# Performance work log

Measured on AMD Instinct MI355X. Metric: run time of the kernel, lower is better.

The kernel has to match this reference:

```python
import jax, jax.numpy as jnp
import numpy as np

N = 100000   # nodes
E = 1600000  # edges (avg degree 16)
DIN, DH, DOUT = 128, 64, 40


def setup_inputs() -> dict:
    key = jax.random.key(0)
    ks = jax.random.split(key, 6)
    x = jax.random.normal(ks[0], (N, DIN), dtype=jnp.float32)
    edge_index = jax.random.randint(ks[1], (2, E), 0, N, dtype=jnp.int32)
    s1 = float(1.0 / np.sqrt(DIN))
    s2 = float(1.0 / np.sqrt(DH))
    W1 = jax.random.uniform(ks[2], (DIN, DH), jnp.float32, -s1, s1)
    b1 = jax.random.uniform(ks[3], (DH,), jnp.float32, -s1, s1)
    W2 = jax.random.uniform(ks[4], (DH, DOUT), jnp.float32, -s2, s2)
    b2 = jax.random.uniform(ks[5], (DOUT,), jnp.float32, -s2, s2)
    return {"x": x, "W1": W1, "b1": b1, "W2": W2, "b2": b2, "edge_index": edge_index}


def _gcn_conv(x, W, b, src, dst):
    """PyG GCNConv: add self-loops, symmetric degree normalization, scatter-add."""
    n = x.shape[0]
    h = x @ W  # [N, F_out] — transform before propagation (PyG order)
    ones = jnp.ones(src.shape[0], dtype=h.dtype)
    deg = jax.ops.segment_sum(ones, dst, num_segments=n) + 1.0  # +1 for self-loop
    dinv = jax.lax.rsqrt(deg)  # deg >= 1, no zero guard needed
    norm = dinv[src] * dinv[dst]  # [E]
    agg = jax.ops.segment_sum(h[src] * norm[:, None], dst, num_segments=n)
    agg = agg + h * (dinv * dinv)[:, None]  # self-loop messages
    return agg + b


def reference(x, W1, b1, W2, b2, edge_index):
    src, dst = edge_index[0], edge_index[1]
    h = jax.nn.relu(_gcn_conv(x, W1, b1, src, dst))
    out = _gcn_conv(h, W2, b2, src, dst)
    return jax.nn.log_softmax(out, axis=1)
```

## Files before the change

### kernel.cpp

```cpp
#include <hip/hip_runtime.h>
#include <hip/hip_fp16.h>
#include <math.h>

#define N_NODES 100000
#define N_EDGES 1600000
#define DIN 128
#define DH 64
#define DOUT 40

#define NB 256
#define BN 391
#define CAP 8192
#define BIN_BLOCKS 256
#define EPB 6250

typedef unsigned short u16;
typedef unsigned int u32;

__device__ inline __half2 u2h(u32 u) {
    union { u32 x; __half2 h; } c; c.x = u; return c.h;
}
__device__ inline u32 h2u(__half2 h) {
    union { __half2 h; u32 x; } c; c.h = h; return c.x;
}


__global__ __launch_bounds__(1024) void k_bin(const int* __restrict__ src,
                                              const int* __restrict__ dst,
                                              int* __restrict__ gcur,
                                              u32* __restrict__ staged) {
    __shared__ int hist[NB];
    __shared__ int base[NB];
    __shared__ int cur[NB];
    int t = threadIdx.x;
    for (int i = t; i < NB; i += 1024) { hist[i] = 0; cur[i] = 0; }
    __syncthreads();
    int e0 = blockIdx.x * EPB;
    int e1 = e0 + EPB; if (e1 > N_EDGES) e1 = N_EDGES;
    for (int e = e0 + t; e < e1; e += 1024)
        atomicAdd(&hist[dst[e] / BN], 1);
    __syncthreads();
    for (int i = t; i < NB; i += 1024) {
        int h = hist[i];
        base[i] = h ? atomicAdd(&gcur[i], h) : 0;
    }
    __syncthreads();
    for (int e = e0 + t; e < e1; e += 1024) {
        int d = dst[e], s = src[e];
        int b = d / BN;
        int dl = d - b * BN;
        int r = base[b] + atomicAdd(&cur[b], 1);
        if (r < CAP) staged[(size_t)b * CAP + r] = (u32)s | ((u32)dl << 17);
    }
}


__global__ __launch_bounds__(256) void k_csr(const int* __restrict__ gcur,
                                             const u32* __restrict__ staged,
                                             int* __restrict__ csr,
                                             int4* __restrict__ meta,
                                             float* __restrict__ dinv) {
    __shared__ u32 sedge[CAP];
    __shared__ int lcsr[CAP];
    __shared__ int hist[BN];
    __shared__ int lrs[BN];
    __shared__ int cur[BN];
    __shared__ int sbuf[256];
    int b = blockIdx.x, t = threadIdx.x;

    int part = 0;
    for (int i = t; i < b; i += 256) {
        int c = gcur[i]; if (c > CAP) c = CAP;
        part += c;
    }
    sbuf[t] = part;
    __syncthreads();
    for (int off = 128; off; off >>= 1) {
        if (t < off) sbuf[t] += sbuf[t + off];
        __syncthreads();
    }
    int base_ = sbuf[0];
    __syncthreads();

    int cnt = gcur[b]; if (cnt > CAP) cnt = CAP;
    for (int i = t; i < BN; i += 256) hist[i] = 0;
    for (int i = t; i < cnt; i += 256) sedge[i] = staged[(size_t)b * CAP + i];
    __syncthreads();
    for (int i = t; i < cnt; i += 256) atomicAdd(&hist[sedge[i] >> 17], 1);
    __syncthreads();

    int v0 = (2 * t < BN) ? hist[2 * t] : 0;
    int v1 = (2 * t + 1 < BN) ? hist[2 * t + 1] : 0;
    int s = v0 + v1;
    sbuf[t] = s;
    __syncthreads();
    for (int off = 1; off < 256; off <<= 1) {
        int add = (t >= off) ? sbuf[t - off] : 0;
        __syncthreads();
        sbuf[t] += add;
        __syncthreads();
    }
    int excl = sbuf[t] - s;
    if (2 * t < BN)     { lrs[2 * t] = excl;      cur[2 * t] = excl; }
    if (2 * t + 1 < BN) { lrs[2 * t + 1] = excl + v0; cur[2 * t + 1] = excl + v0; }
    __syncthreads();

    for (int i = t; i < cnt; i += 256) {
        u32 p = sedge[i];
        int pos = atomicAdd(&cur[p >> 17], 1);
        lcsr[pos] = (int)(p & 0x1FFFF);
    }
    __syncthreads();

    for (int i = t; i < cnt; i += 256) csr[base_ + i] = lcsr[i];
    int n0 = b * BN;
    for (int i = t; i < BN; i += 256) {
        int n = n0 + i;
        if (n < N_NODES) {
            int dg = hist[i];
            float dv = rsqrtf((float)dg + 1.0f);
            meta[n] = make_int4(base_ + lrs[i], dg, __float_as_int(dv), 0);
            dinv[n] = dv;
        }
    }
}


__global__ __launch_bounds__(256) void k_gemm1(const float* __restrict__ x,
                                               const float* __restrict__ W1,
                                               const float* __restrict__ dinv,
                                               u16* __restrict__ h1s) {
    __shared__ float xs[64 * 140];
    __shared__ float wsh[DIN * DH];
    int t = threadIdx.x;
    int row0 = blockIdx.x * 64;

    for (int it = 0; it < 8; ++it) {
        int idx = (it * 256 + t) * 4;
        int r = idx >> 7, c = idx & 127;
        float4 v = make_float4(0.f, 0.f, 0.f, 0.f);
        if (row0 + r < N_NODES) v = *(const float4*)&x[(size_t)(row0 + r) * DIN + c];
        *(float4*)&xs[r * 140 + c] = v;
    }
    for (int it = 0; it < 8; ++it) {
        int idx = (it * 256 + t) * 4;
        *(float4*)&wsh[idx] = *(const float4*)&W1[idx];
    }
    __syncthreads();

    int tr = t & 15;
    int tc = t >> 4;
    float acc[4][4] = {};
    for (int kb = 0; kb < DIN; kb += 4) {
        float4 w0 = *(const float4*)&wsh[(kb + 0) * DH + tr * 4];
        float4 w1 = *(const float4*)&wsh[(kb + 1) * DH + tr * 4];
        float4 w2 = *(const float4*)&wsh[(kb + 2) * DH + tr * 4];
        float4 w3 = *(const float4*)&wsh[(kb + 3) * DH + tr * 4];
#pragma unroll
        for (int i = 0; i < 4; ++i) {
            float4 xv = *(const float4*)&xs[(tc * 4 + i) * 140 + kb];
            acc[i][0] += xv.x * w0.x; acc[i][1] += xv.x * w0.y;
            acc[i][2] += xv.x * w0.z; acc[i][3] += xv.x * w0.w;
            acc[i][0] += xv.y * w1.x; acc[i][1] += xv.y * w1.y;
            acc[i][2] += xv.y * w1.z; acc[i][3] += xv.y * w1.w;
            acc[i][0] += xv.z * w2.x; acc[i][1] += xv.z * w2.y;
            acc[i][2] += xv.z * w2.z; acc[i][3] += xv.z * w2.w;
            acc[i][0] += xv.w * w3.x; acc[i][1] += xv.w * w3.y;
            acc[i][2] += xv.w * w3.z; acc[i][3] += xv.w * w3.w;
        }
    }
#pragma unroll
    for (int i = 0; i < 4; ++i) {
        int row = row0 + tc * 4 + i;
        if (row < N_NODES) {
            float dv = dinv[row];
            ushort4 o;
            o.x = __half_as_ushort(__float2half(acc[i][0] * dv));
            o.y = __half_as_ushort(__float2half(acc[i][1] * dv));
            o.z = __half_as_ushort(__float2half(acc[i][2] * dv));
            o.w = __half_as_ushort(__float2half(acc[i][3] * dv));
            *(ushort4*)&h1s[(size_t)row * DH + tr * 4] = o;
        }
    }
}


__global__ __launch_bounds__(256) void k_agg1(const u16* __restrict__ h1s,
                                              const int4* __restrict__ meta,
                                              const int* __restrict__ csr,
                                              const float* __restrict__ b1,
                                              u16* __restrict__ h1f) {
    int node = blockIdx.x * 4 + (threadIdx.x >> 6);
    if (node >= N_NODES) return;
    node = __builtin_amdgcn_readfirstlane(node);
    int lane = threadIdx.x & 63;
    int es = lane >> 3, fq = lane & 7;
    int4 me = meta[node];
    int s0 = me.x, d = me.y;
    float dv = __int_as_float(me.z);
    const uint4* rows = (const uint4*)h1s;
    __half2 A0 = __float2half2_rn(0.f), A1 = A0, A2 = A0, A3 = A0;
    if (es == 0) {
        uint4 v = rows[(u32)(node * 8 + fq)];
        A0 = u2h(v.x); A1 = u2h(v.y); A2 = u2h(v.z); A3 = u2h(v.w);
    }
    for (int base = 0; base < d; base += 64) {
        int nn = d - base; if (nn > 64) nn = 64;
        int myidx = (lane < nn) ? csr[s0 + base + lane] : 0;
        int j = 0;
        for (; j + 16 <= nn; j += 16) {
            int x0 = __builtin_amdgcn_ds_bpermute((j + es) * 4, myidx);
            int x1 = __builtin_amdgcn_ds_bpermute((j + 8 + es) * 4, myidx);
            uint4 v0 = rows[(u32)(x0 * 8 + fq)];
            uint4 v1 = rows[(u32)(x1 * 8 + fq)];
            A0 = __hadd2(A0, u2h(v0.x)); A1 = __hadd2(A1, u2h(v0.y));
            A2 = __hadd2(A2, u2h(v0.z)); A3 = __hadd2(A3, u2h(v0.w));
            A0 = __hadd2(A0, u2h(v1.x)); A1 = __hadd2(A1, u2h(v1.y));
            A2 = __hadd2(A2, u2h(v1.z)); A3 = __hadd2(A3, u2h(v1.w));
        }
        for (; j < nn; j += 8) {
            int x = __builtin_amdgcn_ds_bpermute((j + es) * 4, myidx);
            if (j + es < nn) {
                uint4 v = rows[(u32)(x * 8 + fq)];
                A0 = __hadd2(A0, u2h(v.x)); A1 = __hadd2(A1, u2h(v.y));
                A2 = __hadd2(A2, u2h(v.z)); A3 = __hadd2(A3, u2h(v.w));
            }
        }
    }
#pragma unroll
    for (int off = 8; off <= 32; off <<= 1) {
        A0 = __hadd2(A0, u2h((u32)__shfl_xor((int)h2u(A0), off, 64)));
        A1 = __hadd2(A1, u2h((u32)__shfl_xor((int)h2u(A1), off, 64)));
        A2 = __hadd2(A2, u2h((u32)__shfl_xor((int)h2u(A2), off, 64)));
        A3 = __hadd2(A3, u2h((u32)__shfl_xor((int)h2u(A3), off, 64)));
    }
    if (es == 0) {
        float4 bva = ((const float4*)b1)[fq * 2 + 0];
        float4 bvb = ((const float4*)b1)[fq * 2 + 1];
        float f0 = fmaxf(__low2float(A0)  * dv + bva.x, 0.f);
        float f1 = fmaxf(__high2float(A0) * dv + bva.y, 0.f);
        float f2 = fmaxf(__low2float(A1)  * dv + bva.z, 0.f);
        float f3 = fmaxf(__high2float(A1) * dv + bva.w, 0.f);
        float f4 = fmaxf(__low2float(A2)  * dv + bvb.x, 0.f);
        float f5 = fmaxf(__high2float(A2) * dv + bvb.y, 0.f);
        float f6 = fmaxf(__low2float(A3)  * dv + bvb.z, 0.f);
        float f7 = fmaxf(__high2float(A3) * dv + bvb.w, 0.f);
        uint4 ov;
        ov.x = h2u(__floats2half2_rn(f0, f1));
        ov.y = h2u(__floats2half2_rn(f2, f3));
        ov.z = h2u(__floats2half2_rn(f4, f5));
        ov.w = h2u(__floats2half2_rn(f6, f7));
        ((uint4*)h1f)[(u32)(node * 8 + fq)] = ov;
    }
}


__global__ __launch_bounds__(256) void k_gemm2(const u16* __restrict__ h1f,
                                               const float* __restrict__ W2,
                                               const float* __restrict__ dinv,
                                               u16* __restrict__ h2s) {
    __shared__ float xs[64 * 68];
    __shared__ float wsh[DH * DOUT];
    int t = threadIdx.x;
    int row0 = blockIdx.x * 64;

    for (int it = 0; it < 4; ++it) {
        int idx = (it * 256 + t) * 4;
        int r = idx >> 6, c = idx & 63;
        float4 v = make_float4(0.f, 0.f, 0.f, 0.f);
        if (row0 + r < N_NODES) {
            uint2 hv = *(const uint2*)&h1f[(size_t)(row0 + r) * DH + c];
            __half2 hlo = u2h(hv.x), hhi = u2h(hv.y);
            v = make_float4(__low2float(hlo), __high2float(hlo),
                            __low2float(hhi), __high2float(hhi));
        }
        *(float4*)&xs[r * 68 + c] = v;
    }
    for (int idx = t * 4; idx < DH * DOUT; idx += 1024) {
        *(float4*)&wsh[idx] = *(const float4*)&W2[idx];
    }
    __syncthreads();

    int fg = t & 7;
    int rg = t >> 3;
    float acc[2][5] = {};
    for (int k = 0; k < DH; ++k) {
        float x0 = xs[(rg * 2 + 0) * 68 + k];
        float x1 = xs[(rg * 2 + 1) * 68 + k];
#pragma unroll
        for (int j = 0; j < 5; ++j) {
            float w = wsh[k * DOUT + fg * 5 + j];
            acc[0][j] += x0 * w;
            acc[1][j] += x1 * w;
        }
    }
#pragma unroll
    for (int i = 0; i < 2; ++i) {
        int row = row0 + rg * 2 + i;
        if (row < N_NODES) {
            float dvv = dinv[row];
#pragma unroll
            for (int j = 0; j < 5; ++j)
                h2s[(size_t)row * DOUT + fg * 5 + j] =
                    __half_as_ushort(__float2half(acc[i][j] * dvv));
        }
    }
}


__global__ __launch_bounds__(256) void k_agg2(const u16* __restrict__ h2s,
                                              const int4* __restrict__ meta,
                                              const int* __restrict__ csr,
                                              const float* __restrict__ b2,
                                              float* __restrict__ out) {
    int node = blockIdx.x * 4 + (threadIdx.x >> 6);
    if (node >= N_NODES) return;
    node = __builtin_amdgcn_readfirstlane(node);
    int lane = threadIdx.x & 63;
    int es = lane >> 3, fq = lane & 7;
    bool act = fq < 5;
    int4 me = meta[node];
    int s0 = me.x, d = me.y;
    float dv = __int_as_float(me.z);
    const uint4* rows = (const uint4*)h2s;
    __half2 A0 = __float2half2_rn(0.f), A1 = A0, A2 = A0, A3 = A0;
    if (es == 0 && act) {
        uint4 v = rows[(u32)(node * 5 + fq)];
        A0 = u2h(v.x); A1 = u2h(v.y); A2 = u2h(v.z); A3 = u2h(v.w);
    }
    for (int base = 0; base < d; base += 64) {
        int nn = d - base; if (nn > 64) nn = 64;
        int myidx = (lane < nn) ? csr[s0 + base + lane] : 0;
        int j = 0;
        for (; j + 16 <= nn; j += 16) {
            int x0 = __builtin_amdgcn_ds_bpermute((j + es) * 4, myidx);
            int x1 = __builtin_amdgcn_ds_bpermute((j + 8 + es) * 4, myidx);
            if (act) {
                uint4 v0 = rows[(u32)(x0 * 5 + fq)];
                uint4 v1 = rows[(u32)(x1 * 5 + fq)];
                A0 = __hadd2(A0, u2h(v0.x)); A1 = __hadd2(A1, u2h(v0.y));
                A2 = __hadd2(A2, u2h(v0.z)); A3 = __hadd2(A3, u2h(v0.w));
                A0 = __hadd2(A0, u2h(v1.x)); A1 = __hadd2(A1, u2h(v1.y));
                A2 = __hadd2(A2, u2h(v1.z)); A3 = __hadd2(A3, u2h(v1.w));
            }
        }
        for (; j < nn; j += 8) {
            int x = __builtin_amdgcn_ds_bpermute((j + es) * 4, myidx);
            if (act && j + es < nn) {
                uint4 v = rows[(u32)(x * 5 + fq)];
                A0 = __hadd2(A0, u2h(v.x)); A1 = __hadd2(A1, u2h(v.y));
                A2 = __hadd2(A2, u2h(v.z)); A3 = __hadd2(A3, u2h(v.w));
            }
        }
    }
#pragma unroll
    for (int off = 8; off <= 32; off <<= 1) {
        A0 = __hadd2(A0, u2h((u32)__shfl_xor((int)h2u(A0), off, 64)));
        A1 = __hadd2(A1, u2h((u32)__shfl_xor((int)h2u(A1), off, 64)));
        A2 = __hadd2(A2, u2h((u32)__shfl_xor((int)h2u(A2), off, 64)));
        A3 = __hadd2(A3, u2h((u32)__shfl_xor((int)h2u(A3), off, 64)));
    }

    float4 bva = act ? ((const float4*)b2)[fq * 2 + 0] : make_float4(0.f, 0.f, 0.f, 0.f);
    float4 bvb = act ? ((const float4*)b2)[fq * 2 + 1] : make_float4(0.f, 0.f, 0.f, 0.f);
    float v0 = act ? __low2float(A0)  * dv + bva.x : -INFINITY;
    float v1 = act ? __high2float(A0) * dv + bva.y : -INFINITY;
    float v2 = act ? __low2float(A1)  * dv + bva.z : -INFINITY;
    float v3 = act ? __high2float(A1) * dv + bva.w : -INFINITY;
    float v4 = act ? __low2float(A2)  * dv + bvb.x : -INFINITY;
    float v5 = act ? __high2float(A2) * dv + bvb.y : -INFINITY;
    float v6 = act ? __low2float(A3)  * dv + bvb.z : -INFINITY;
    float v7 = act ? __high2float(A3) * dv + bvb.w : -INFINITY;
    float m = fmaxf(fmaxf(fmaxf(v0, v1), fmaxf(v2, v3)),
                    fmaxf(fmaxf(v4, v5), fmaxf(v6, v7)));
    m = fmaxf(m, __shfl_xor(m, 1, 64));
    m = fmaxf(m, __shfl_xor(m, 2, 64));
    m = fmaxf(m, __shfl_xor(m, 4, 64));
    float ex = 0.f;
    if (act) {
        ex = __expf(v0 - m) + __expf(v1 - m) + __expf(v2 - m) + __expf(v3 - m)
           + __expf(v4 - m) + __expf(v5 - m) + __expf(v6 - m) + __expf(v7 - m);
    }
    ex += __shfl_xor(ex, 1, 64);
    ex += __shfl_xor(ex, 2, 64);
    ex += __shfl_xor(ex, 4, 64);
    float lse = m + __logf(ex);
    if (es == 0 && act) {
        float4 oa = make_float4(v0 - lse, v1 - lse, v2 - lse, v3 - lse);
        float4 ob = make_float4(v4 - lse, v5 - lse, v6 - lse, v7 - lse);
        *(float4*)&out[(u32)(node * 40 + fq * 8 + 0)] = oa;
        *(float4*)&out[(u32)(node * 40 + fq * 8 + 4)] = ob;
    }
}


extern "C" void kernel_launch(void* const* d_in, const int* in_sizes, int n_in,
                              void* d_out, int out_size, void* d_ws, size_t ws_size,
                              hipStream_t stream) {
    const float* x  = (const float*)d_in[0];
    const float* W1 = (const float*)d_in[1];
    const float* b1 = (const float*)d_in[2];
    const float* W2 = (const float*)d_in[3];
    const float* b2 = (const float*)d_in[4];
    const int* eidx = (const int*)d_in[5];
    const int* srcp = eidx;
    const int* dstp = eidx + N_EDGES;
    float* out = (float*)d_out;

    char* w = (char*)d_ws;
    int* gcur    = (int*)w;   w += sizeof(int) * NB;
    float* dinv  = (float*)w; w += sizeof(float) * N_NODES + 48;
    int4* meta   = (int4*)w;  w += sizeof(int4) * N_NODES;
    u32* staged  = (u32*)w;   w += sizeof(u32) * (size_t)NB * CAP;
    int* csr     = (int*)w;   w += sizeof(int) * N_EDGES;
    u16* h1s     = (u16*)w;   w += sizeof(u16) * (size_t)N_NODES * DH;
    u16* h1f     = (u16*)w;   w += sizeof(u16) * (size_t)N_NODES * DH;
    u16* h2s     = h1s;

    hipMemsetAsync(gcur, 0, sizeof(int) * NB, stream);
    k_bin<<<BIN_BLOCKS, 1024, 0, stream>>>(srcp, dstp, gcur, staged);
    k_csr<<<NB, 256, 0, stream>>>(gcur, staged, csr, meta, dinv);
    k_gemm1<<<(N_NODES + 63) / 64, 256, 0, stream>>>(x, W1, dinv, h1s);
    k_agg1<<<(N_NODES + 3) / 4, 256, 0, stream>>>(h1s, meta, csr, b1, h1f);
    k_gemm2<<<(N_NODES + 63) / 64, 256, 0, stream>>>(h1f, W2, dinv, h2s);
    k_agg2<<<(N_NODES + 3) / 4, 256, 0, stream>>>(h2s, meta, csr, b2, out);
}
```

Baseline: 202.2 us.

## Fuse second-layer GEMM into first aggregation kernel via wave shuffles

Merges the layer-1 aggregation with the layer-2 dense transform. After each wave finishes reducing a node's 64-wide hidden vector, it applies bias and ReLU and multiplies by W2, which is held in shared memory, using shuffles to broadcast hidden values. The h2 row is then written directly. This removes the h1f intermediate write and re-read and one kernel launch. In exchange, every block of only 4 nodes reloads W2 (10 KB) into LDS and adds a barrier, and the per-lane matvec runs 64 serial shuffle+FMA steps.

```diff
diff --git a/kernel.cpp b/kernel.cpp
--- a/kernel.cpp
+++ b/kernel.cpp
@@ -185,15 +185,23 @@
 }
 
 
-__global__ __launch_bounds__(256) void k_agg1(const u16* __restrict__ h1s,
-                                              const int4* __restrict__ meta,
-                                              const int* __restrict__ csr,
-                                              const float* __restrict__ b1,
-                                              u16* __restrict__ h1f) {
-    int node = blockIdx.x * 4 + (threadIdx.x >> 6);
-    if (node >= N_NODES) return;
+__global__ __launch_bounds__(256) void k_agg1f(const u16* __restrict__ h1s,
+                                               const int4* __restrict__ meta,
+                                               const int* __restrict__ csr,
+                                               const float* __restrict__ b1,
+                                               const float* __restrict__ W2,
+                                               u16* __restrict__ h2s) {
+    __shared__ float w2s[DH * DOUT];
+    int t = threadIdx.x;
+    for (int idx = t * 4; idx < DH * DOUT; idx += 1024)
+        *(float4*)&w2s[idx] = *(const float4*)&W2[idx];
+    __syncthreads();
+
+    int node = blockIdx.x * 4 + (t >> 6);
+    bool valid = node < N_NODES;
+    if (!valid) node = N_NODES - 1;
     node = __builtin_amdgcn_readfirstlane(node);
-    int lane = threadIdx.x & 63;
+    int lane = t & 63;
     int es = lane >> 3, fq = lane & 7;
     int4 me = meta[node];
     int s0 = me.x, d = me.y;
@@ -234,77 +242,29 @@
         A2 = __hadd2(A2, u2h((u32)__shfl_xor((int)h2u(A2), off, 64)));
         A3 = __hadd2(A3, u2h((u32)__shfl_xor((int)h2u(A3), off, 64)));
     }
-    if (es == 0) {
-        float4 bva = ((const float4*)b1)[fq * 2 + 0];
-        float4 bvb = ((const float4*)b1)[fq * 2 + 1];
-        float f0 = fmaxf(__low2float(A0)  * dv + bva.x, 0.f);
-        float f1 = fmaxf(__high2float(A0) * dv + bva.y, 0.f);
-        float f2 = fmaxf(__low2float(A1)  * dv + bva.z, 0.f);
-        float f3 = fmaxf(__high2float(A1) * dv + bva.w, 0.f);
-        float f4 = fmaxf(__low2float(A2)  * dv + bvb.x, 0.f);
-        float f5 = fmaxf(__high2float(A2) * dv + bvb.y, 0.f);
-        float f6 = fmaxf(__low2float(A3)  * dv + bvb.z, 0.f);
-        float f7 = fmaxf(__high2float(A3) * dv + bvb.w, 0.f);
-        uint4 ov;
-        ov.x = h2u(__floats2half2_rn(f0, f1));
-        ov.y = h2u(__floats2half2_rn(f2, f3));
-        ov.z = h2u(__floats2half2_rn(f4, f5));
-        ov.w = h2u(__floats2half2_rn(f6, f7));
-        ((uint4*)h1f)[(u32)(node * 8 + fq)] = ov;
-    }
-}
-
-
-__global__ __launch_bounds__(256) void k_gemm2(const u16* __restrict__ h1f,
-                                               const float* __restrict__ W2,
-                                               const float* __restrict__ dinv,
-                                               u16* __restrict__ h2s) {
-    __shared__ float xs[64 * 68];
-    __shared__ float wsh[DH * DOUT];
-    int t = threadIdx.x;
-    int row0 = blockIdx.x * 64;
-
-    for (int it = 0; it < 4; ++it) {
-        int idx = (it * 256 + t) * 4;
-        int r = idx >> 6, c = idx & 63;
-        float4 v = make_float4(0.f, 0.f, 0.f, 0.f);
-        if (row0 + r < N_NODES) {
-            uint2 hv = *(const uint2*)&h1f[(size_t)(row0 + r) * DH + c];
-            __half2 hlo = u2h(hv.x), hhi = u2h(hv.y);
-            v = make_float4(__low2float(hlo), __high2float(hlo),
-                            __low2float(hhi), __high2float(hhi));
-        }
-        *(float4*)&xs[r * 68 + c] = v;
-    }
-    for (int idx = t * 4; idx < DH * DOUT; idx += 1024) {
-        *(float4*)&wsh[idx] = *(const float4*)&W2[idx];
-    }
-    __syncthreads();
-
-    int fg = t & 7;
-    int rg = t >> 3;
-    float acc[2][5] = {};
+
+    float4 bva = ((const float4*)b1)[fq * 2 + 0];
+    float4 bvb = ((const float4*)b1)[fq * 2 + 1];
+    float f[8];
+    f[0] = fmaxf(__low2float(A0)  * dv + bva.x, 0.f);
+    f[1] = fmaxf(__high2float(A0) * dv + bva.y, 0.f);
+    f[2] = fmaxf(__low2float(A1)  * dv + bva.z, 0.f);
+    f[3] = fmaxf(__high2float(A1) * dv + bva.w, 0.f);
+    f[4] = fmaxf(__low2float(A2)  * dv + bvb.x, 0.f);
+    f[5] = fmaxf(__high2float(A2) * dv + bvb.y, 0.f);
+    f[6] = fmaxf(__low2float(A3)  * dv + bvb.z, 0.f);
+    f[7] = fmaxf(__high2float(A3) * dv + bvb.w, 0.f);
+
+    int jj = (lane < DOUT) ? lane : 0;
+    float acc = 0.f;
+#pragma unroll
     for (int k = 0; k < DH; ++k) {
-        float x0 = xs[(rg * 2 + 0) * 68 + k];
-        float x1 = xs[(rg * 2 + 1) * 68 + k];
-#pragma unroll
-        for (int j = 0; j < 5; ++j) {
-            float w = wsh[k * DOUT + fg * 5 + j];
-            acc[0][j] += x0 * w;
-            acc[1][j] += x1 * w;
-        }
-    }
-#pragma unroll
-    for (int i = 0; i < 2; ++i) {
-        int row = row0 + rg * 2 + i;
-        if (row < N_NODES) {
-            float dvv = dinv[row];
-#pragma unroll
-            for (int j = 0; j < 5; ++j)
-                h2s[(size_t)row * DOUT + fg * 5 + j] =
-                    __half_as_ushort(__float2half(acc[i][j] * dvv));
-        }
-    }
+        float hk = __shfl(f[k & 7], k >> 3, 64);
+        acc += hk * w2s[k * DOUT + jj];
+    }
+    if (valid && lane < DOUT)
+        h2s[(u32)(node * DOUT + lane)] =
+            __half_as_ushort(__float2half(acc * dv));
 }
 
 
@@ -414,14 +374,12 @@
     u32* staged  = (u32*)w;   w += sizeof(u32) * (size_t)NB * CAP;
     int* csr     = (int*)w;   w += sizeof(int) * N_EDGES;
     u16* h1s     = (u16*)w;   w += sizeof(u16) * (size_t)N_NODES * DH;
-    u16* h1f     = (u16*)w;   w += sizeof(u16) * (size_t)N_NODES * DH;
-    u16* h2s     = h1s;
+    u16* h2s     = (u16*)w;   w += sizeof(u16) * (size_t)N_NODES * DOUT;
 
     hipMemsetAsync(gcur, 0, sizeof(int) * NB, stream);
     k_bin<<<BIN_BLOCKS, 1024, 0, stream>>>(srcp, dstp, gcur, staged);
     k_csr<<<NB, 256, 0, stream>>>(gcur, staged, csr, meta, dinv);
     k_gemm1<<<(N_NODES + 63) / 64, 256, 0, stream>>>(x, W1, dinv, h1s);
-    k_agg1<<<(N_NODES + 3) / 4, 256, 0, stream>>>(h1s, meta, csr, b1, h1f);
-    k_gemm2<<<(N_NODES + 63) / 64, 256, 0, stream>>>(h1f, W2, dinv, h2s);
+    k_agg1f<<<(N_NODES + 3) / 4, 256, 0, stream>>>(h1s, meta, csr, b1, W2, h2s);
     k_agg2<<<(N_NODES + 3) / 4, 256, 0, stream>>>(h2s, meta, csr, b2, out);
 }
```

Measured after the change: 223.7 us. +10.7%, slower.

## Merge CSR build and first GEMM into one launch using global degree counts

Applied to the files above, without the earlier changes.

The CSR-building kernel and the first dense transform are combined into a single launch, with blocks split by index into CSR blocks and GEMM blocks. The GEMM no longer has to wait for the CSR kernel's dinv, so k_bin now also counts per-node degree with global atomics and the GEMM recomputes rsqrt from it. This removes one kernel boundary and lets the GEMM overlap with the CSR pass. In exchange it adds 1.6M global atomics in the binning kernel, and the 71 KB of shared memory now reserved by every block may lower occupancy for the GEMM blocks.

```diff
diff --git a/kernel.cpp b/kernel.cpp
--- a/kernel.cpp
+++ b/kernel.cpp
@@ -13,6 +13,7 @@
 #define CAP 8192
 #define BIN_BLOCKS 256
 #define EPB 6250
+#define GEMM1_BLOCKS ((N_NODES + 63) / 64)
 
 typedef unsigned short u16;
 typedef unsigned int u32;
@@ -28,6 +29,7 @@
 __global__ __launch_bounds__(1024) void k_bin(const int* __restrict__ src,
                                               const int* __restrict__ dst,
                                               int* __restrict__ gcur,
+                                              int* __restrict__ deg,
                                               u32* __restrict__ staged) {
     __shared__ int hist[NB];
     __shared__ int base[NB];
@@ -37,8 +39,11 @@
     __syncthreads();
     int e0 = blockIdx.x * EPB;
     int e1 = e0 + EPB; if (e1 > N_EDGES) e1 = N_EDGES;
-    for (int e = e0 + t; e < e1; e += 1024)
-        atomicAdd(&hist[dst[e] / BN], 1);
+    for (int e = e0 + t; e < e1; e += 1024) {
+        int dd = dst[e];
+        atomicAdd(&hist[dd / BN], 1);
+        atomicAdd(&deg[dd], 1);
+    }
     __syncthreads();
     for (int i = t; i < NB; i += 1024) {
         int h = hist[i];
@@ -55,131 +60,134 @@
 }
 
 
-__global__ __launch_bounds__(256) void k_csr(const int* __restrict__ gcur,
+__global__ __launch_bounds__(256) void k_mid(const int* __restrict__ gcur,
                                              const u32* __restrict__ staged,
                                              int* __restrict__ csr,
                                              int4* __restrict__ meta,
-                                             float* __restrict__ dinv) {
-    __shared__ u32 sedge[CAP];
-    __shared__ int lcsr[CAP];
-    __shared__ int hist[BN];
-    __shared__ int lrs[BN];
-    __shared__ int cur[BN];
-    __shared__ int sbuf[256];
-    int b = blockIdx.x, t = threadIdx.x;
-
-    int part = 0;
-    for (int i = t; i < b; i += 256) {
-        int c = gcur[i]; if (c > CAP) c = CAP;
-        part += c;
-    }
-    sbuf[t] = part;
-    __syncthreads();
-    for (int off = 128; off; off >>= 1) {
-        if (t < off) sbuf[t] += sbuf[t + off];
-        __syncthreads();
-    }
-    int base_ = sbuf[0];
-    __syncthreads();
-
-    int cnt = gcur[b]; if (cnt > CAP) cnt = CAP;
-    for (int i = t; i < BN; i += 256) hist[i] = 0;
-    for (int i = t; i < cnt; i += 256) sedge[i] = staged[(size_t)b * CAP + i];
-    __syncthreads();
-    for (int i = t; i < cnt; i += 256) atomicAdd(&hist[sedge[i] >> 17], 1);
-    __syncthreads();
-
-    int v0 = (2 * t < BN) ? hist[2 * t] : 0;
-    int v1 = (2 * t + 1 < BN) ? hist[2 * t + 1] : 0;
-    int s = v0 + v1;
-    sbuf[t] = s;
-    __syncthreads();
-    for (int off = 1; off < 256; off <<= 1) {
-        int add = (t >= off) ? sbuf[t - off] : 0;
-        __syncthreads();
-        sbuf[t] += add;
-        __syncthreads();
-    }
-    int excl = sbuf[t] - s;
-    if (2 * t < BN)     { lrs[2 * t] = excl;      cur[2 * t] = excl; }
-    if (2 * t + 1 < BN) { lrs[2 * t + 1] = excl + v0; cur[2 * t + 1] = excl + v0; }
-    __syncthreads();
-
-    for (int i = t; i < cnt; i += 256) {
-        u32 p = sedge[i];
-        int pos = atomicAdd(&cur[p >> 17], 1);
-        lcsr[pos] = (int)(p & 0x1FFFF);
-    }
-    __syncthreads();
-
-    for (int i = t; i < cnt; i += 256) csr[base_ + i] = lcsr[i];
-    int n0 = b * BN;
-    for (int i = t; i < BN; i += 256) {
-        int n = n0 + i;
-        if (n < N_NODES) {
-            int dg = hist[i];
-            float dv = rsqrtf((float)dg + 1.0f);
-            meta[n] = make_int4(base_ + lrs[i], dg, __float_as_int(dv), 0);
-            dinv[n] = dv;
-        }
-    }
-}
-
-
-__global__ __launch_bounds__(256) void k_gemm1(const float* __restrict__ x,
-                                               const float* __restrict__ W1,
-                                               const float* __restrict__ dinv,
-                                               u16* __restrict__ h1s) {
-    __shared__ float xs[64 * 140];
-    __shared__ float wsh[DIN * DH];
+                                             float* __restrict__ dinv,
+                                             const int* __restrict__ deg,
+                                             const float* __restrict__ x,
+                                             const float* __restrict__ W1,
+                                             u16* __restrict__ h1s) {
+    __shared__ __align__(16) char smem[71296];
     int t = threadIdx.x;
-    int row0 = blockIdx.x * 64;
-
-    for (int it = 0; it < 8; ++it) {
-        int idx = (it * 256 + t) * 4;
-        int r = idx >> 7, c = idx & 127;
-        float4 v = make_float4(0.f, 0.f, 0.f, 0.f);
-        if (row0 + r < N_NODES) v = *(const float4*)&x[(size_t)(row0 + r) * DIN + c];
-        *(float4*)&xs[r * 140 + c] = v;
-    }
-    for (int it = 0; it < 8; ++it) {
-        int idx = (it * 256 + t) * 4;
-        *(float4*)&wsh[idx] = *(const float4*)&W1[idx];
-    }
-    __syncthreads();
-
-    int tr = t & 15;
-    int tc = t >> 4;
-    float acc[4][4] = {};
-    for (int kb = 0; kb < DIN; kb += 4) {
-        float4 w0 = *(const float4*)&wsh[(kb + 0) * DH + tr * 4];
-        float4 w1 = *(const float4*)&wsh[(kb + 1) * DH + tr * 4];
-        float4 w2 = *(const float4*)&wsh[(kb + 2) * DH + tr * 4];
-        float4 w3 = *(const float4*)&wsh[(kb + 3) * DH + tr * 4];
+    int blk = blockIdx.x;
+
+    if (blk < NB) {
+        u32* sedge = (u32*)smem;
+        int* lcsr  = (int*)(smem + 32768);
+        int* hist  = (int*)(smem + 65536);
+        int* lrs   = (int*)(smem + 67100);
+        int* cur   = (int*)(smem + 68664);
+        int* sbuf  = (int*)(smem + 70228);
+        int b = blk;
+
+        int part = 0;
+        for (int i = t; i < b; i += 256) {
+            int c = gcur[i]; if (c > CAP) c = CAP;
+            part += c;
+        }
+        sbuf[t] = part;
+        __syncthreads();
+        for (int off = 128; off; off >>= 1) {
+            if (t < off) sbuf[t] += sbuf[t + off];
+            __syncthreads();
+        }
+        int base_ = sbuf[0];
+        __syncthreads();
+
+        int cnt = gcur[b]; if (cnt > CAP) cnt = CAP;
+        for (int i = t; i < BN; i += 256) hist[i] = 0;
+        for (int i = t; i < cnt; i += 256) sedge[i] = staged[(size_t)b * CAP + i];
+        __syncthreads();
+        for (int i = t; i < cnt; i += 256) atomicAdd(&hist[sedge[i] >> 17], 1);
+        __syncthreads();
+
+        int v0 = (2 * t < BN) ? hist[2 * t] : 0;
+        int v1 = (2 * t + 1 < BN) ? hist[2 * t + 1] : 0;
+        int s = v0 + v1;
+        sbuf[t] = s;
+        __syncthreads();
+        for (int off = 1; off < 256; off <<= 1) {
+            int add = (t >= off) ? sbuf[t - off] : 0;
+            __syncthreads();
+            sbuf[t] += add;
+            __syncthreads();
+        }
+        int excl = sbuf[t] - s;
+        if (2 * t < BN)     { lrs[2 * t] = excl;          cur[2 * t] = excl; }
+        if (2 * t + 1 < BN) { lrs[2 * t + 1] = excl + v0; cur[2 * t + 1] = excl + v0; }
+        __syncthreads();
+
+        for (int i = t; i < cnt; i += 256) {
+            u32 p = sedge[i];
+            int pos = atomicAdd(&cur[p >> 17], 1);
+            lcsr[pos] = (int)(p & 0x1FFFF);
+        }
+        __syncthreads();
+
+        for (int i = t; i < cnt; i += 256) csr[base_ + i] = lcsr[i];
+        int n0 = b * BN;
+        for (int i = t; i < BN; i += 256) {
+            int n = n0 + i;
+            if (n < N_NODES) {
+                int dg = hist[i];
+                float dv = rsqrtf((float)dg + 1.0f);
+                meta[n] = make_int4(base_ + lrs[i], dg, __float_as_int(dv), 0);
+                dinv[n] = dv;
+            }
+        }
+    } else {
+        float* xs  = (float*)smem;
+        float* wsh = (float*)(smem + 35840);
+        int row0 = (blk - NB) * 64;
+
+        for (int it = 0; it < 8; ++it) {
+            int idx = (it * 256 + t) * 4;
+            int r = idx >> 7, c = idx & 127;
+            float4 v = make_float4(0.f, 0.f, 0.f, 0.f);
+            if (row0 + r < N_NODES) v = *(const float4*)&x[(size_t)(row0 + r) * DIN + c];
+            *(float4*)&xs[r * 140 + c] = v;
+        }
+        for (int it = 0; it < 8; ++it) {
+            int idx = (it * 256 + t) * 4;
+            *(float4*)&wsh[idx] = *(const float4*)&W1[idx];
+        }
+        __syncthreads();
+
+        int tr = t & 15;
+        int tc = t >> 4;
+        float acc[4][4] = {};
+        for (int kb = 0; kb < DIN; kb += 4) {
+            float4 w0 = *(const float4*)&wsh[(kb + 0) * DH + tr * 4];
+            float4 w1 = *(const float4*)&wsh[(kb + 1) * DH + tr * 4];
+            float4 w2 = *(const float4*)&wsh[(kb + 2) * DH + tr * 4];
+            float4 w3 = *(const float4*)&wsh[(kb + 3) * DH + tr * 4];
+#pragma unroll
+            for (int i = 0; i < 4; ++i) {
+                float4 xv = *(const float4*)&xs[(tc * 4 + i) * 140 + kb];
+                acc[i][0] += xv.x * w0.x; acc[i][1] += xv.x * w0.y;
+                acc[i][2] += xv.x * w0.z; acc[i][3] += xv.x * w0.w;
+                acc[i][0] += xv.y * w1.x; acc[i][1] += xv.y * w1.y;
+                acc[i][2] += xv.y * w1.z; acc[i][3] += xv.y * w1.w;
+                acc[i][0] += xv.z * w2.x; acc[i][1] += xv.z * w2.y;
+                acc[i][2] += xv.z * w2.z; acc[i][3] += xv.z * w2.w;
+                acc[i][0] += xv.w * w3.x; acc[i][1] += xv.w * w3.y;
+                acc[i][2] += xv.w * w3.z; acc[i][3] += xv.w * w3.w;
+            }
+        }
 #pragma unroll
         for (int i = 0; i < 4; ++i) {
-            float4 xv = *(const float4*)&xs[(tc * 4 + i) * 140 + kb];
-            acc[i][0] += xv.x * w0.x; acc[i][1] += xv.x * w0.y;
-            acc[i][2] += xv.x * w0.z; acc[i][3] += xv.x * w0.w;
-            acc[i][0] += xv.y * w1.x; acc[i][1] += xv.y * w1.y;
-            acc[i][2] += xv.y * w1.z; acc[i][3] += xv.y * w1.w;
-            acc[i][0] += xv.z * w2.x; acc[i][1] += xv.z * w2.y;
-            acc[i][2] += xv.z * w2.z; acc[i][3] += xv.z * w2.w;
-            acc[i][0] += xv.w * w3.x; acc[i][1] += xv.w * w3.y;
-            acc[i][2] += xv.w * w3.z; acc[i][3] += xv.w * w3.w;
-        }
-    }
-#pragma unroll
-    for (int i = 0; i < 4; ++i) {
-        int row = row0 + tc * 4 + i;
-        if (row < N_NODES) {
-            float dv = dinv[row];
-            ushort4 o;
-            o.x = __half_as_ushort(__float2half(acc[i][0] * dv));
-            o.y = __half_as_ushort(__float2half(acc[i][1] * dv));
-            o.z = __half_as_ushort(__float2half(acc[i][2] * dv));
-            o.w = __half_as_ushort(__float2half(acc[i][3] * dv));
-            *(ushort4*)&h1s[(size_t)row * DH + tr * 4] = o;
+            int row = row0 + tc * 4 + i;
+            if (row < N_NODES) {
+                float dv = rsqrtf((float)deg[row] + 1.0f);
+                ushort4 o;
+                o.x = __half_as_ushort(__float2half(acc[i][0] * dv));
+                o.y = __half_as_ushort(__float2half(acc[i][1] * dv));
+                o.z = __half_as_ushort(__float2half(acc[i][2] * dv));
+                o.w = __half_as_ushort(__float2half(acc[i][3] * dv));
+                *(ushort4*)&h1s[(size_t)row * DH + tr * 4] = o;
+            }
         }
     }
 }
@@ -409,6 +417,7 @@
 
     char* w = (char*)d_ws;
     int* gcur    = (int*)w;   w += sizeof(int) * NB;
+    int* deg     = (int*)w;   w += sizeof(int) * N_NODES;
     float* dinv  = (float*)w; w += sizeof(float) * N_NODES + 48;
     int4* meta   = (int4*)w;  w += sizeof(int4) * N_NODES;
     u32* staged  = (u32*)w;   w += sizeof(u32) * (size_t)NB * CAP;
@@ -417,10 +426,10 @@
     u16* h1f     = (u16*)w;   w += sizeof(u16) * (size_t)N_NODES * DH;
     u16* h2s     = h1s;
 
-    hipMemsetAsync(gcur, 0, sizeof(int) * NB, stream);
-    k_bin<<<BIN_BLOCKS, 1024, 0, stream>>>(srcp, dstp, gcur, staged);
-    k_csr<<<NB, 256, 0, stream>>>(gcur, staged, csr, meta, dinv);
-    k_gemm1<<<(N_NODES + 63) / 64, 256, 0, stream>>>(x, W1, dinv, h1s);
+    hipMemsetAsync(gcur, 0, sizeof(int) * (NB + N_NODES), stream);
+    k_bin<<<BIN_BLOCKS, 1024, 0, stream>>>(srcp, dstp, gcur, deg, staged);
+    k_mid<<<NB + GEMM1_BLOCKS, 256, 0, stream>>>(gcur, staged, csr, meta, dinv,
+                                                 deg, x, W1, h1s);
     k_agg1<<<(N_NODES + 3) / 4, 256, 0, stream>>>(h1s, meta, csr, b1, h1f);
     k_gemm2<<<(N_NODES + 63) / 64, 256, 0, stream>>>(h1f, W2, dinv, h2s);
     k_agg2<<<(N_NODES + 3) / 4, 256, 0, stream>>>(h2s, meta, csr, b2, out);
```

New measurement: 256.0 us. 1.27x slower.
